# Optimization experiments

Measured on AMD Instinct MI355X. Metric: run time of the kernel, lower is better.

The kernel has to match this reference:

```python
import jax, jax.numpy as jnp
import numpy as np

TEMPERATURE = 8.0  # sqrt(head_dim=64)
NEG_INF = -1e9


def setup_inputs() -> dict:
    key = jax.random.key(0)
    k1, k2, k3, k4, k5 = jax.random.split(key, 5)
    B, H, S, D = 1, 8, 2048, 64
    q = jax.random.normal(k1, (B, H, S, D), dtype=jnp.float32)
    k = jax.random.normal(k2, (B, H, S, D), dtype=jnp.float32)
    v = jax.random.normal(k3, (B, H, S, D), dtype=jnp.float32)
    sph = jax.random.uniform(k4, (B, H, S, S), dtype=jnp.float32)
    mask = jax.random.randint(k5, (B, H, S, S), 0, 2, dtype=jnp.int32)
    return {"q": q, "k": k, "v": v, "sph": sph, "mask": mask}


def reference(q, k, v, sph, mask):
    # scores: [B,H,Sq,Sk]
    attn = jnp.einsum('bhqd,bhkd->bhqk', q / TEMPERATURE, k)
    attn = attn * sph                       # multiplicative bias
    attn = jnp.where(mask == 0, NEG_INF, attn)
    p_attn = jax.nn.softmax(attn, axis=-1)  # dropout p=0 -> identity
    out = jnp.einsum('bhqk,bhkd->bhqd', p_attn, v)
    return (out, p_attn)
```

## Files before the change

kernel.cpp:

```cpp
#include <hip/hip_runtime.h>

#define SLEN 2048
#define DIM  64
#define NH   8
#define TQ   16
#define NEG_INF -1e9f

typedef __attribute__((ext_vector_type(8))) short short8;
typedef __attribute__((ext_vector_type(4))) float f32x4;
typedef unsigned short ushort;

__device__ inline ushort f2bf(float x) {
    unsigned u = __float_as_uint(x);
    u += 0x7fffu + ((u >> 16) & 1u);
    return (ushort)(u >> 16);
}
__device__ inline float bf2f(ushort b) {
    return __uint_as_float(((unsigned)b) << 16);
}

__global__ __launch_bounds__(256)
void convk_kernel(const float* __restrict__ k,
                  ushort* __restrict__ khi, ushort* __restrict__ klo)
{
    int i4 = blockIdx.x * 256 + threadIdx.x;
    float4 x = ((const float4*)k)[i4];
    ushort h0 = f2bf(x.x), h1 = f2bf(x.y), h2 = f2bf(x.z), h3 = f2bf(x.w);
    ushort4 hi = {h0, h1, h2, h3};
    ushort4 lo = {f2bf(x.x - bf2f(h0)), f2bf(x.y - bf2f(h1)),
                  f2bf(x.z - bf2f(h2)), f2bf(x.w - bf2f(h3))};
    ((ushort4*)khi)[i4] = hi;
    ((ushort4*)klo)[i4] = lo;
}

__global__ __launch_bounds__(256)
void convv_kernel(const float* __restrict__ v, ushort* __restrict__ vt)
{
    __shared__ ushort sT[64][70];
    const int h  = blockIdx.x >> 5;
    const int st = blockIdx.x & 31;
    const int t  = threadIdx.x;
    {
        const int r0 = t >> 4;
        const int c  = (t & 15) * 4;
        #pragma unroll
        for (int rr = r0; rr < 64; rr += 16) {
            float4 x = *(const float4*)(v + ((size_t)(h * SLEN + st * 64 + rr)) * DIM + c);
            sT[c + 0][rr] = f2bf(x.x);
            sT[c + 1][rr] = f2bf(x.y);
            sT[c + 2][rr] = f2bf(x.z);
            sT[c + 3][rr] = f2bf(x.w);
        }
    }
    __syncthreads();
    {
        const int d  = t >> 2;
        const int s0 = (t & 3) * 16;
        short8 a = *(const short8*)(&sT[d][s0]);
        short8 b = *(const short8*)(&sT[d][s0 + 8]);
        ushort* dst = vt + ((size_t)(h * DIM + d)) * SLEN + st * 64 + s0;
        *(short8*)(dst)     = a;
        *(short8*)(dst + 8) = b;
    }
}

__global__ __launch_bounds__(512, 2)
void attn_mfma_kernel(const float* __restrict__ q,
                      const ushort* __restrict__ khi,
                      const ushort* __restrict__ klo,
                      const ushort* __restrict__ vt,
                      const float* __restrict__ sph,
                      const int*   __restrict__ mask,
                      float* __restrict__ out,
                      float* __restrict__ p_out)
{
    __shared__ ushort sP[TQ][SLEN + 8];
    __shared__ ushort sQhi[TQ][72];
    __shared__ ushort sQlo[TQ][72];
    __shared__ float sMax[TQ][8];
    __shared__ float sSum[TQ][8];
    __shared__ float sC[4][TQ][16];

    const int tid  = threadIdx.x;
    const int wave = tid >> 6;
    const int lane = tid & 63;
    const int quad = lane >> 4;
    const int l16  = lane & 15;
    const int bx   = blockIdx.x;
    const int h    = bx >> 7;
    const int qr0  = (bx & 127) * TQ;

    {
        int e = tid * 2;
        int r = e >> 6, d = e & 63;
        float2 qv = *(const float2*)(q + ((size_t)(h * SLEN + qr0 + r)) * DIM + d);
        ushort h0 = f2bf(qv.x), h1 = f2bf(qv.y);
        sQhi[r][d]     = h0;
        sQhi[r][d + 1] = h1;
        sQlo[r][d]     = f2bf(qv.x - bf2f(h0));
        sQlo[r][d + 1] = f2bf(qv.y - bf2f(h1));
    }
    __syncthreads();

    short8 ah0 = *(const short8*)(&sQhi[l16][quad * 8]);
    short8 ah1 = *(const short8*)(&sQhi[l16][32 + quad * 8]);
    short8 al0 = *(const short8*)(&sQlo[l16][quad * 8]);
    short8 al1 = *(const short8*)(&sQlo[l16][32 + quad * 8]);

    const int n0 = wave * 256;

    f32x4 c[16];
    #pragma unroll
    for (int t = 0; t < 16; ++t) c[t] = (f32x4){0.f, 0.f, 0.f, 0.f};

    #pragma unroll
    for (int t = 0; t < 16; ++t) {
        const size_t rowb = ((size_t)(h * SLEN + n0 + t * 16 + l16)) * DIM + quad * 8;
        short8 bh0 = *(const short8*)(khi + rowb);
        short8 bh1 = *(const short8*)(khi + rowb + 32);
        short8 bl0 = *(const short8*)(klo + rowb);
        short8 bl1 = *(const short8*)(klo + rowb + 32);
        c[t] = __builtin_amdgcn_mfma_f32_16x16x32_bf16(ah0, bh0, c[t], 0, 0, 0);
        c[t] = __builtin_amdgcn_mfma_f32_16x16x32_bf16(ah1, bh1, c[t], 0, 0, 0);
        c[t] = __builtin_amdgcn_mfma_f32_16x16x32_bf16(ah0, bl0, c[t], 0, 0, 0);
        c[t] = __builtin_amdgcn_mfma_f32_16x16x32_bf16(ah1, bl1, c[t], 0, 0, 0);
        c[t] = __builtin_amdgcn_mfma_f32_16x16x32_bf16(al0, bh0, c[t], 0, 0, 0);
        c[t] = __builtin_amdgcn_mfma_f32_16x16x32_bf16(al1, bh1, c[t], 0, 0, 0);
    }

    size_t rowb[4];
    #pragma unroll
    for (int j = 0; j < 4; ++j)
        rowb[j] = ((size_t)(h * SLEN) + qr0 + quad * 4 + j) * SLEN + n0 + l16;

    float rmax[4] = {-3.4e38f, -3.4e38f, -3.4e38f, -3.4e38f};
    #pragma unroll
    for (int half = 0; half < 2; ++half) {
        float sv[32];
        int   mv[32];
        #pragma unroll
        for (int u = 0; u < 32; ++u) {
            const int t = half * 8 + (u >> 2), j = u & 3;
            sv[u] = __builtin_nontemporal_load(sph  + rowb[j] + t * 16);
            mv[u] = __builtin_nontemporal_load(mask + rowb[j] + t * 16);
        }
        #pragma unroll
        for (int u = 0; u < 32; ++u) {
            const int t = half * 8 + (u >> 2), j = u & 3;
            float s = c[t][j] * 0.125f * sv[u];
            s = (mv[u] == 0) ? NEG_INF : s;
            c[t][j] = s;
            rmax[j] = fmaxf(rmax[j], s);
        }
    }
    #pragma unroll
    for (int off = 1; off <= 8; off <<= 1) {
        #pragma unroll
        for (int j = 0; j < 4; ++j)
            rmax[j] = fmaxf(rmax[j], __shfl_xor(rmax[j], off));
    }
    if (l16 == 0) {
        #pragma unroll
        for (int j = 0; j < 4; ++j) sMax[quad * 4 + j][wave] = rmax[j];
    }
    __syncthreads();

    float M[4];
    #pragma unroll
    for (int j = 0; j < 4; ++j) {
        float m = sMax[quad * 4 + j][0];
        #pragma unroll
        for (int w = 1; w < 8; ++w) m = fmaxf(m, sMax[quad * 4 + j][w]);
        M[j] = m;
    }

    float rsum[4] = {0.f, 0.f, 0.f, 0.f};
    #pragma unroll
    for (int t = 0; t < 16; ++t) {
        #pragma unroll
        for (int j = 0; j < 4; ++j) {
            float e = __expf(c[t][j] - M[j]);
            c[t][j] = e;
            rsum[j] += e;
        }
    }
    #pragma unroll
    for (int off = 1; off <= 8; off <<= 1) {
        #pragma unroll
        for (int j = 0; j < 4; ++j)
            rsum[j] += __shfl_xor(rsum[j], off);
    }
    if (l16 == 0) {
        #pragma unroll
        for (int j = 0; j < 4; ++j) sSum[quad * 4 + j][wave] = rsum[j];
    }
    __syncthreads();

    float inv[4];
    #pragma unroll
    for (int j = 0; j < 4; ++j) {
        float s = 0.f;
        #pragma unroll
        for (int w = 0; w < 8; ++w) s += sSum[quad * 4 + j][w];
        inv[j] = 1.0f / s;
    }

    #pragma unroll
    for (int t = 0; t < 16; ++t) {
        #pragma unroll
        for (int j = 0; j < 4; ++j) {
            const int row = quad * 4 + j;
            const int col = n0 + t * 16 + l16;
            float p = c[t][j] * inv[j];
            __builtin_nontemporal_store(p, p_out + rowb[j] + t * 16);
            sP[row][col] = f2bf(p);
        }
    }
    __syncthreads();

    const int ntile = wave & 3;
    const int khalf = wave >> 2;
    f32x4 o = (f32x4){0.f, 0.f, 0.f, 0.f};
    const ushort* vb = vt + ((size_t)(h * DIM + ntile * 16 + l16)) * SLEN
                          + khalf * 1024 + quad * 8;
    #pragma unroll 8
    for (int s = 0; s < 32; ++s) {
        short8 a = *(const short8*)(&sP[l16][khalf * 1024 + s * 32 + quad * 8]);
        short8 b = *(const short8*)(vb + s * 32);
        o = __builtin_amdgcn_mfma_f32_16x16x32_bf16(a, b, o, 0, 0, 0);
    }
    if (wave >= 4) {
        #pragma unroll
        for (int j = 0; j < 4; ++j) sC[ntile][quad * 4 + j][l16] = o[j];
    }
    __syncthreads();
    if (wave < 4) {
        #pragma unroll
        for (int j = 0; j < 4; ++j) {
            float r = o[j] + sC[ntile][quad * 4 + j][l16];
            __builtin_nontemporal_store(
                r, out + ((size_t)(h * SLEN) + qr0 + quad * 4 + j) * DIM + ntile * 16 + l16);
        }
    }
}

extern "C" void kernel_launch(void* const* d_in, const int* in_sizes, int n_in,
                              void* d_out, int out_size, void* d_ws, size_t ws_size,
                              hipStream_t stream) {
    const float* q    = (const float*)d_in[0];
    const float* k    = (const float*)d_in[1];
    const float* v    = (const float*)d_in[2];
    const float* sph  = (const float*)d_in[3];
    const int*   mask = (const int*)d_in[4];
    float* out   = (float*)d_out;
    float* p_out = out + (size_t)NH * SLEN * DIM;

    const size_t nkv = (size_t)NH * SLEN * DIM;
    ushort* khi = (ushort*)d_ws;
    ushort* klo = khi + nkv;
    ushort* vt  = klo + nkv;

    hipLaunchKernelGGL(convk_kernel, dim3(nkv / 4 / 256), dim3(256), 0, stream,
                       k, khi, klo);
    hipLaunchKernelGGL(convv_kernel, dim3(NH * (SLEN / 64)), dim3(256), 0, stream,
                       v, vt);
    hipLaunchKernelGGL(attn_mfma_kernel, dim3(NH * (SLEN / TQ)), dim3(512), 0, stream,
                       q, khi, klo, vt, sph, mask, out, p_out);
}
```

Measured before the change: 417.6 us.

## Transpose QK MFMA operands for vectorized sph/mask loads, fuse conversion kernels

Swaps the A/B operands of the QK^T MFMA so each lane holds four consecutive key columns of one query row. The sph and mask reads and the p_attn writes then become 16-byte vector accesses instead of scalar strided ones, which targets the dominant 2048x2048 memory streams. The row max and sum reductions shrink to two cross-lane shuffles. The K and V conversion kernels are merged into one launch, the block-to-head mapping is interleaved, and the p_attn store is moved after the PV MFMA to overlap with it. The merged conversion kernel calls __syncthreads inside a block-uniform branch, and the sP bf16 writes now use a different LDS access pattern.

```diff
diff --git a/kernel.cpp b/kernel.cpp
--- a/kernel.cpp
+++ b/kernel.cpp
@@ -7,7 +7,9 @@
 #define NEG_INF -1e9f
 
 typedef __attribute__((ext_vector_type(8))) short short8;
+typedef __attribute__((ext_vector_type(4))) short short4v;
 typedef __attribute__((ext_vector_type(4))) float f32x4;
+typedef __attribute__((ext_vector_type(4))) int   i32x4;
 typedef unsigned short ushort;
 
 __device__ inline ushort f2bf(float x) {
@@ -20,27 +22,26 @@
 }
 
 __global__ __launch_bounds__(256)
-void convk_kernel(const float* __restrict__ k,
-                  ushort* __restrict__ khi, ushort* __restrict__ klo)
-{
-    int i4 = blockIdx.x * 256 + threadIdx.x;
-    float4 x = ((const float4*)k)[i4];
-    ushort h0 = f2bf(x.x), h1 = f2bf(x.y), h2 = f2bf(x.z), h3 = f2bf(x.w);
-    ushort4 hi = {h0, h1, h2, h3};
-    ushort4 lo = {f2bf(x.x - bf2f(h0)), f2bf(x.y - bf2f(h1)),
-                  f2bf(x.z - bf2f(h2)), f2bf(x.w - bf2f(h3))};
-    ((ushort4*)khi)[i4] = hi;
-    ((ushort4*)klo)[i4] = lo;
-}
-
-__global__ __launch_bounds__(256)
-void convv_kernel(const float* __restrict__ v, ushort* __restrict__ vt)
+void conv_kernel(const float* __restrict__ k, const float* __restrict__ v,
+                 ushort* __restrict__ khi, ushort* __restrict__ klo,
+                 ushort* __restrict__ vt)
 {
     __shared__ ushort sT[64][70];
-    const int h  = blockIdx.x >> 5;
-    const int st = blockIdx.x & 31;
+    const int bx = blockIdx.x;
     const int t  = threadIdx.x;
     {
+        int i4 = bx * 256 + t;
+        float4 x = ((const float4*)k)[i4];
+        ushort h0 = f2bf(x.x), h1 = f2bf(x.y), h2 = f2bf(x.z), h3 = f2bf(x.w);
+        ushort4 hi = {h0, h1, h2, h3};
+        ushort4 lo = {f2bf(x.x - bf2f(h0)), f2bf(x.y - bf2f(h1)),
+                      f2bf(x.z - bf2f(h2)), f2bf(x.w - bf2f(h3))};
+        ((ushort4*)khi)[i4] = hi;
+        ((ushort4*)klo)[i4] = lo;
+    }
+    if (bx < 256) {
+        const int h  = bx >> 5;
+        const int st = bx & 31;
         const int r0 = t >> 4;
         const int c  = (t & 15) * 4;
         #pragma unroll
@@ -51,9 +52,7 @@
             sT[c + 2][rr] = f2bf(x.z);
             sT[c + 3][rr] = f2bf(x.w);
         }
-    }
-    __syncthreads();
-    {
+        __syncthreads();
         const int d  = t >> 2;
         const int s0 = (t & 3) * 16;
         short8 a = *(const short8*)(&sT[d][s0]);
@@ -87,8 +86,8 @@
     const int quad = lane >> 4;
     const int l16  = lane & 15;
     const int bx   = blockIdx.x;
-    const int h    = bx >> 7;
-    const int qr0  = (bx & 127) * TQ;
+    const int h    = bx & 7;
+    const int qr0  = (bx >> 3) * TQ;
 
     {
         int e = tid * 2;
@@ -102,10 +101,10 @@
     }
     __syncthreads();
 
-    short8 ah0 = *(const short8*)(&sQhi[l16][quad * 8]);
-    short8 ah1 = *(const short8*)(&sQhi[l16][32 + quad * 8]);
-    short8 al0 = *(const short8*)(&sQlo[l16][quad * 8]);
-    short8 al1 = *(const short8*)(&sQlo[l16][32 + quad * 8]);
+    short8 qh0 = *(const short8*)(&sQhi[l16][quad * 8]);
+    short8 qh1 = *(const short8*)(&sQhi[l16][32 + quad * 8]);
+    short8 ql0 = *(const short8*)(&sQlo[l16][quad * 8]);
+    short8 ql1 = *(const short8*)(&sQlo[l16][32 + quad * 8]);
 
     const int n0 = wave * 256;
 
@@ -115,106 +114,76 @@
 
     #pragma unroll
     for (int t = 0; t < 16; ++t) {
-        const size_t rowb = ((size_t)(h * SLEN + n0 + t * 16 + l16)) * DIM + quad * 8;
-        short8 bh0 = *(const short8*)(khi + rowb);
-        short8 bh1 = *(const short8*)(khi + rowb + 32);
-        short8 bl0 = *(const short8*)(klo + rowb);
-        short8 bl1 = *(const short8*)(klo + rowb + 32);
-        c[t] = __builtin_amdgcn_mfma_f32_16x16x32_bf16(ah0, bh0, c[t], 0, 0, 0);
-        c[t] = __builtin_amdgcn_mfma_f32_16x16x32_bf16(ah1, bh1, c[t], 0, 0, 0);
-        c[t] = __builtin_amdgcn_mfma_f32_16x16x32_bf16(ah0, bl0, c[t], 0, 0, 0);
-        c[t] = __builtin_amdgcn_mfma_f32_16x16x32_bf16(ah1, bl1, c[t], 0, 0, 0);
-        c[t] = __builtin_amdgcn_mfma_f32_16x16x32_bf16(al0, bh0, c[t], 0, 0, 0);
-        c[t] = __builtin_amdgcn_mfma_f32_16x16x32_bf16(al1, bh1, c[t], 0, 0, 0);
-    }
-
-    size_t rowb[4];
-    #pragma unroll
-    for (int j = 0; j < 4; ++j)
-        rowb[j] = ((size_t)(h * SLEN) + qr0 + quad * 4 + j) * SLEN + n0 + l16;
-
-    float rmax[4] = {-3.4e38f, -3.4e38f, -3.4e38f, -3.4e38f};
-    #pragma unroll
-    for (int half = 0; half < 2; ++half) {
-        float sv[32];
-        int   mv[32];
-        #pragma unroll
-        for (int u = 0; u < 32; ++u) {
-            const int t = half * 8 + (u >> 2), j = u & 3;
-            sv[u] = __builtin_nontemporal_load(sph  + rowb[j] + t * 16);
-            mv[u] = __builtin_nontemporal_load(mask + rowb[j] + t * 16);
-        }
-        #pragma unroll
-        for (int u = 0; u < 32; ++u) {
-            const int t = half * 8 + (u >> 2), j = u & 3;
-            float s = c[t][j] * 0.125f * sv[u];
-            s = (mv[u] == 0) ? NEG_INF : s;
+        const size_t krow = ((size_t)(h * SLEN + n0 + t * 16 + l16)) * DIM + quad * 8;
+        short8 kh0 = *(const short8*)(khi + krow);
+        short8 kh1 = *(const short8*)(khi + krow + 32);
+        short8 kl0 = *(const short8*)(klo + krow);
+        short8 kl1 = *(const short8*)(klo + krow + 32);
+        c[t] = __builtin_amdgcn_mfma_f32_16x16x32_bf16(kh0, qh0, c[t], 0, 0, 0);
+        c[t] = __builtin_amdgcn_mfma_f32_16x16x32_bf16(kh1, qh1, c[t], 0, 0, 0);
+        c[t] = __builtin_amdgcn_mfma_f32_16x16x32_bf16(kh0, ql0, c[t], 0, 0, 0);
+        c[t] = __builtin_amdgcn_mfma_f32_16x16x32_bf16(kh1, ql1, c[t], 0, 0, 0);
+        c[t] = __builtin_amdgcn_mfma_f32_16x16x32_bf16(kl0, qh0, c[t], 0, 0, 0);
+        c[t] = __builtin_amdgcn_mfma_f32_16x16x32_bf16(kl1, qh1, c[t], 0, 0, 0);
+    }
+
+    const size_t prow = ((size_t)(h * SLEN) + qr0 + l16) * SLEN + n0 + quad * 4;
+
+    f32x4 sv[16];
+    i32x4 mv[16];
+    #pragma unroll
+    for (int t = 0; t < 16; ++t) {
+        sv[t] = __builtin_nontemporal_load((const f32x4*)(sph  + prow + t * 16));
+        mv[t] = __builtin_nontemporal_load((const i32x4*)(mask + prow + t * 16));
+    }
+    __builtin_amdgcn_sched_barrier(0);
+
+    float rmax = -3.4e38f;
+    #pragma unroll
+    for (int t = 0; t < 16; ++t) {
+        #pragma unroll
+        for (int j = 0; j < 4; ++j) {
+            float s = c[t][j] * 0.125f * sv[t][j];
+            s = (mv[t][j] == 0) ? NEG_INF : s;
             c[t][j] = s;
-            rmax[j] = fmaxf(rmax[j], s);
-        }
-    }
-    #pragma unroll
-    for (int off = 1; off <= 8; off <<= 1) {
-        #pragma unroll
-        for (int j = 0; j < 4; ++j)
-            rmax[j] = fmaxf(rmax[j], __shfl_xor(rmax[j], off));
-    }
-    if (l16 == 0) {
-        #pragma unroll
-        for (int j = 0; j < 4; ++j) sMax[quad * 4 + j][wave] = rmax[j];
-    }
-    __syncthreads();
-
-    float M[4];
-    #pragma unroll
-    for (int j = 0; j < 4; ++j) {
-        float m = sMax[quad * 4 + j][0];
-        #pragma unroll
-        for (int w = 1; w < 8; ++w) m = fmaxf(m, sMax[quad * 4 + j][w]);
-        M[j] = m;
-    }
-
-    float rsum[4] = {0.f, 0.f, 0.f, 0.f};
+            rmax = fmaxf(rmax, s);
+        }
+    }
+    rmax = fmaxf(rmax, __shfl_xor(rmax, 16));
+    rmax = fmaxf(rmax, __shfl_xor(rmax, 32));
+    if (lane < 16) sMax[l16][wave] = rmax;
+    __syncthreads();
+
+    float M = sMax[l16][0];
+    #pragma unroll
+    for (int w = 1; w < 8; ++w) M = fmaxf(M, sMax[l16][w]);
+
+    float rsum = 0.f;
     #pragma unroll
     for (int t = 0; t < 16; ++t) {
         #pragma unroll
         for (int j = 0; j < 4; ++j) {
-            float e = __expf(c[t][j] - M[j]);
+            float e = __expf(c[t][j] - M);
             c[t][j] = e;
-            rsum[j] += e;
-        }
-    }
-    #pragma unroll
-    for (int off = 1; off <= 8; off <<= 1) {
-        #pragma unroll
-        for (int j = 0; j < 4; ++j)
-            rsum[j] += __shfl_xor(rsum[j], off);
-    }
-    if (l16 == 0) {
-        #pragma unroll
-        for (int j = 0; j < 4; ++j) sSum[quad * 4 + j][wave] = rsum[j];
-    }
-    __syncthreads();
-
-    float inv[4];
-    #pragma unroll
-    for (int j = 0; j < 4; ++j) {
-        float s = 0.f;
-        #pragma unroll
-        for (int w = 0; w < 8; ++w) s += sSum[quad * 4 + j][w];
-        inv[j] = 1.0f / s;
-    }
-
-    #pragma unroll
-    for (int t = 0; t < 16; ++t) {
-        #pragma unroll
-        for (int j = 0; j < 4; ++j) {
-            const int row = quad * 4 + j;
-            const int col = n0 + t * 16 + l16;
-            float p = c[t][j] * inv[j];
-            __builtin_nontemporal_store(p, p_out + rowb[j] + t * 16);
-            sP[row][col] = f2bf(p);
-        }
+            rsum += e;
+        }
+    }
+    rsum += __shfl_xor(rsum, 16);
+    rsum += __shfl_xor(rsum, 32);
+    if (lane < 16) sSum[l16][wave] = rsum;
+    __syncthreads();
+
+    float ssum = 0.f;
+    #pragma unroll
+    for (int w = 0; w < 8; ++w) ssum += sSum[l16][w];
+    const float inv = 1.0f / ssum;
+
+    #pragma unroll
+    for (int t = 0; t < 16; ++t) {
+        short4v pb;
+        #pragma unroll
+        for (int j = 0; j < 4; ++j) pb[j] = (short)f2bf(c[t][j] * inv);
+        *(short4v*)(&sP[l16][n0 + t * 16 + quad * 4]) = pb;
     }
     __syncthreads();
 
@@ -233,13 +202,21 @@
         #pragma unroll
         for (int j = 0; j < 4; ++j) sC[ntile][quad * 4 + j][l16] = o[j];
     }
-    __syncthreads();
+
+    #pragma unroll
+    for (int t = 0; t < 16; ++t) {
+        f32x4 p4;
+        #pragma unroll
+        for (int j = 0; j < 4; ++j) p4[j] = c[t][j] * inv;
+        __builtin_nontemporal_store(p4, (f32x4*)(p_out + prow + t * 16));
+    }
+    __syncthreads();
+
     if (wave < 4) {
         #pragma unroll
         for (int j = 0; j < 4; ++j) {
             float r = o[j] + sC[ntile][quad * 4 + j][l16];
-            __builtin_nontemporal_store(
-                r, out + ((size_t)(h * SLEN) + qr0 + quad * 4 + j) * DIM + ntile * 16 + l16);
+            out[((size_t)(h * SLEN) + qr0 + quad * 4 + j) * DIM + ntile * 16 + l16] = r;
         }
     }
 }
@@ -260,10 +237,8 @@
     ushort* klo = khi + nkv;
     ushort* vt  = klo + nkv;
 
-    hipLaunchKernelGGL(convk_kernel, dim3(nkv / 4 / 256), dim3(256), 0, stream,
-                       k, khi, klo);
-    hipLaunchKernelGGL(convv_kernel, dim3(NH * (SLEN / 64)), dim3(256), 0, stream,
-                       v, vt);
+    hipLaunchKernelGGL(conv_kernel, dim3(nkv / 4 / 256), dim3(256), 0, stream,
+                       k, v, khi, klo, vt);
     hipLaunchKernelGGL(attn_mfma_kernel, dim3(NH * (SLEN / TQ)), dim3(512), 0, stream,
                        q, khi, klo, vt, sph, mask, out, p_out);
 }
```

Result: no change. 419.9 us (+0.6%).
